# Kernel optimization log

Hardware: AMD Instinct MI355X
Metric: run time of the kernel (lower is better)

## Reference

```python
import jax, jax.numpy as jnp
import numpy as np

B, S, D, NB = 8, 8192, 512, 16


def _ln(x, g, b, eps=1e-5):
    m = jnp.mean(x, axis=-1, keepdims=True)
    v = jnp.var(x, axis=-1, keepdims=True)
    return (x - m) / jnp.sqrt(v + eps) * g + b


def setup_inputs() -> dict:
    key = jax.random.key(0)
    ks = jax.random.split(key, 12)
    s = 0.02
    f32 = jnp.float32
    return {
        "emb_input": jax.random.normal(ks[0], (B, S, D), f32),
        "dis_input": jax.random.normal(ks[1], (B, S, D), f32),
        "torsion": jax.random.normal(ks[2], (B, D), f32),
        "dis_unlocked": 1,
        "delay_steps": 3,
        # embodied selector + per-block params (stacked over NB blocks)
        "emb_sel_W": jax.random.normal(ks[3], (D, NB), f32) * s,
        "emb_sel_b": jnp.zeros((NB,), f32),
        "emb_ln_g": jnp.ones((NB, D), f32),
        "emb_ln_b": jnp.zeros((NB, D), f32),
        "emb_w1": jax.random.normal(ks[4], (NB, D, D), f32) * s,
        "emb_b1": jnp.zeros((NB, D), f32),
        "emb_w2": jax.random.normal(ks[5], (NB, D, D), f32) * s,
        "emb_b2": jnp.zeros((NB, D), f32),
        # disembodied selector + per-block params
        "dis_sel_W": jax.random.normal(ks[6], (D, NB), f32) * s,
        "dis_sel_b": jnp.zeros((NB,), f32),
        "dis_ln1_g": jnp.ones((NB, D), f32),
        "dis_ln1_b": jnp.zeros((NB, D), f32),
        "dis_attn_W": jax.random.normal(ks[7], (NB, D, D), f32) * s,
        "dis_attn_b": jnp.zeros((NB, D), f32),
        "dis_ln2_g": jnp.ones((NB, D), f32),
        "dis_ln2_b": jnp.zeros((NB, D), f32),
        "dis_ff1_W": jax.random.normal(ks[8], (NB, D, 2 * D), f32) * s,
        "dis_ff1_b": jnp.zeros((NB, 2 * D), f32),
        "dis_ff2_W": jax.random.normal(ks[9], (NB, 2 * D, D), f32) * s,
        "dis_ff2_b": jnp.zeros((NB, D), f32),
    }


def reference(emb_input, dis_input, torsion, dis_unlocked, delay_steps,
              emb_sel_W, emb_sel_b, emb_ln_g, emb_ln_b, emb_w1, emb_b1, emb_w2, emb_b2,
              dis_sel_W, dis_sel_b, dis_ln1_g, dis_ln1_b, dis_attn_W, dis_attn_b,
              dis_ln2_g, dis_ln2_b, dis_ff1_W, dis_ff1_b, dis_ff2_W, dis_ff2_b):
    # ---- embodied branch: sigmoid-gated top-2 routing (indices from batch elem 0)
    scores = jax.nn.sigmoid(jnp.mean(emb_input, axis=1) @ emb_sel_W + emb_sel_b)  # [B,NB]
    _, top = jax.lax.top_k(scores[0], 2)
    t_emb = 1.0 + torsion[:, None, :] * 0.1  # [B,1,D]
    h = emb_input
    for i in range(2):  # fixed top-2, unrolled; block params gathered dynamically
        idx = top[i]
        hn = _ln(h, emb_ln_g[idx], emb_ln_b[idx])
        hn = jnp.tanh(hn @ emb_w1[idx] + emb_b1[idx]) @ emb_w2[idx] + emb_b2[idx]
        h = h + hn * t_emb * 0.3
    emb_h = h

    # ---- disembodied branch (dis_unlocked is a static Python int)
    dis_h = None
    if dis_unlocked:
        delayed = jnp.mean(dis_input, axis=1)  # [B,D]; single-write buffer returns current mean
        dscores = jax.nn.sigmoid(delayed @ dis_sel_W + dis_sel_b)
        _, dtop = jax.lax.top_k(dscores[0], 2)
        t_dis = 1.0 + torsion[:, None, :] * 0.05
        dh = dis_input
        for i in range(2):
            idx = dtop[i]
            h1 = _ln(dh, dis_ln1_g[idx], dis_ln1_b[idx])
            h1 = h1 @ dis_attn_W[idx] + dis_attn_b[idx]
            h1 = (h1 + delayed[:, None, :] * 0.2) * t_dis
            hm = dh + h1 * 0.5
            h2 = _ln(hm, dis_ln2_g[idx], dis_ln2_b[idx])
            h2 = jax.nn.gelu(h2 @ dis_ff1_W[idx] + dis_ff1_b[idx], approximate=False)
            h2 = h2 @ dis_ff2_W[idx] + dis_ff2_b[idx]
            dh = hm + h2 * 0.5
        dis_h = dh
    return (emb_h, dis_h)
```

## Files before the change

kernel.cpp:

```cpp
#include <hip/hip_runtime.h>
#include <stdint.h>

#define B_  8
#define S_  8192
#define D_  512
#define NB_ 16
#define M_  (B_*S_)

typedef short bf16x8 __attribute__((ext_vector_type(8)));
typedef float f32x4  __attribute__((ext_vector_type(4)));

static __device__ __forceinline__ unsigned short f2bf(float f) {
  unsigned int u = __float_as_uint(f);
  u += 0x7fff + ((u >> 16) & 1);
  return (unsigned short)(u >> 16);
}

__global__ __launch_bounds__(256) void zero_kernel(float* p, int n) {
  int i = blockIdx.x * 256 + threadIdx.x;
  if (i < n) p[i] = 0.f;
}

__global__ __launch_bounds__(512) void colmean_kernel(const float* __restrict__ x,
                                                      float* __restrict__ acc) {
  int b = blockIdx.x, d = threadIdx.x;
  const float* p = x + ((size_t)b * S_ + (size_t)blockIdx.y * 512) * D_ + d;
  float s = 0.f;
  #pragma unroll 8
  for (int i = 0; i < 512; i++) s += p[(size_t)i * D_];
  atomicAdd(&acc[b * D_ + d], s);
}

__global__ __launch_bounds__(128) void top2_kernel(const float* __restrict__ embAcc,
                                                   const float* __restrict__ embW,
                                                   const float* __restrict__ embB,
                                                   const float* __restrict__ disAcc,
                                                   const float* __restrict__ disW,
                                                   const float* __restrict__ disB,
                                                   int* __restrict__ out) {
  int wave = threadIdx.x >> 6, lane = threadIdx.x & 63;
  const float* acc = wave ? disAcc : embAcc;
  const float* W   = wave ? disW   : embW;
  const float* bb  = wave ? disB   : embB;
  const float invS = 1.f / (float)S_;
  float logit[NB_];
  for (int nb = 0; nb < NB_; nb++) {
    float s = 0.f;
    for (int d = lane; d < D_; d += 64) s += acc[d] * invS * W[d * NB_ + nb];
    for (int o = 32; o; o >>= 1) s += __shfl_xor(s, o);
    logit[nb] = s + bb[nb];
  }
  if (lane == 0) {
    int i0 = 0;
    for (int i = 1; i < NB_; i++) if (logit[i] > logit[i0]) i0 = i;
    int i1 = (i0 == 0) ? 1 : 0;
    for (int i = 0; i < NB_; i++) if (i != i0 && logit[i] > logit[i1]) i1 = i;
    out[wave * 2 + 0] = i0;
    out[wave * 2 + 1] = i1;
  }
}

__global__ __launch_bounds__(256) void ln_cast_kernel(const float* __restrict__ x,
                                                      const float* __restrict__ gB,
                                                      const float* __restrict__ bB,
                                                      const int* __restrict__ idxPtr,
                                                      unsigned short* __restrict__ out) {
  int row  = blockIdx.x * 4 + (threadIdx.x >> 6);
  int lane = threadIdx.x & 63;
  const float4* xr = (const float4*)(x + (size_t)row * D_ + lane * 8);
  float4 v0 = xr[0], v1 = xr[1];
  float s  = v0.x + v0.y + v0.z + v0.w + v1.x + v1.y + v1.z + v1.w;
  float sq = v0.x*v0.x + v0.y*v0.y + v0.z*v0.z + v0.w*v0.w
           + v1.x*v1.x + v1.y*v1.y + v1.z*v1.z + v1.w*v1.w;
  for (int o = 32; o; o >>= 1) { s += __shfl_xor(s, o); sq += __shfl_xor(sq, o); }
  float mean = s * (1.f / D_);
  float var  = sq * (1.f / D_) - mean * mean;
  float rstd = rsqrtf(var + 1e-5f);
  int idx = *idxPtr;
  const float4* g4 = (const float4*)(gB + (size_t)idx * D_ + lane * 8);
  const float4* b4 = (const float4*)(bB + (size_t)idx * D_ + lane * 8);
  float4 g0 = g4[0], g1 = g4[1], c0 = b4[0], c1 = b4[1];
  float xv[8] = {v0.x, v0.y, v0.z, v0.w, v1.x, v1.y, v1.z, v1.w};
  float gv[8] = {g0.x, g0.y, g0.z, g0.w, g1.x, g1.y, g1.z, g1.w};
  float bv[8] = {c0.x, c0.y, c0.z, c0.w, c1.x, c1.y, c1.z, c1.w};
  unsigned short o8[8] __attribute__((aligned(16)));
  #pragma unroll
  for (int k = 0; k < 8; k++) o8[k] = f2bf((xv[k] - mean) * rstd * gv[k] + bv[k]);
  *(uint4*)(out + (size_t)row * D_ + lane * 8) = *(const uint4*)o8;
}

__global__ __launch_bounds__(256) void wconvert_kernel(const float* __restrict__ srcAll,
                                                       const int* __restrict__ idxPtr,
                                                       int K, int N,
                                                       unsigned short* __restrict__ dst) {
  __shared__ float t[32][33];
  int idx = *idxPtr;
  const float* src = srcAll + (size_t)idx * K * N;
  int k0 = blockIdx.y * 32, n0 = blockIdx.x * 32;
  int tid = threadIdx.x;
  int kl = tid >> 5, nl = tid & 31;
  #pragma unroll
  for (int r = 0; r < 4; r++)
    t[kl + r * 8][nl] = src[(size_t)(k0 + kl + r * 8) * N + n0 + nl];
  __syncthreads();
  #pragma unroll
  for (int r = 0; r < 4; r++)
    dst[(size_t)(n0 + kl + r * 8) * K + k0 + nl] = f2bf(t[nl][kl + r * 8]);
}

template<int EPI>
__global__ __launch_bounds__(256) void gemm_kernel(const unsigned short* __restrict__ A,
                                                   const unsigned short* __restrict__ Bt,
                                                   int K, int N,
                                                   const int* __restrict__ idxPtr,
                                                   const float* __restrict__ biasBase,
                                                   const float* __restrict__ hin,
                                                   float* __restrict__ fout,
                                                   unsigned short* __restrict__ bout,
                                                   const float* __restrict__ torsion,
                                                   const float* __restrict__ dAcc) {
  __shared__ __align__(16) unsigned short As[128 * 32];
  __shared__ __align__(16) unsigned short Bs[128 * 32];
  const int tid  = threadIdx.x;
  const int wave = tid >> 6, lane = tid & 63;
  const int quad = lane >> 4, l16 = lane & 15;
  const int wm = (wave >> 1) * 64, wn = (wave & 1) * 64;
  const int m0 = blockIdx.x * 128, n0 = blockIdx.y * 128;
  const int r0  = tid >> 2;
  const int seg = (tid & 3) * 8;
  const unsigned short* Ag = A  + (size_t)(m0 + r0) * K + seg;
  const unsigned short* Bg = Bt + (size_t)(n0 + r0) * K + seg;

  f32x4 acc[4][4] = {};
  for (int kt = 0; kt < K; kt += 32) {
    uint4 a0 = *(const uint4*)(Ag + kt);
    uint4 a1 = *(const uint4*)(Ag + (size_t)64 * K + kt);
    uint4 b0 = *(const uint4*)(Bg + kt);
    uint4 b1 = *(const uint4*)(Bg + (size_t)64 * K + kt);
    *(uint4*)(&As[(size_t)r0 * 32 + seg])        = a0;
    *(uint4*)(&As[(size_t)(r0 + 64) * 32 + seg]) = a1;
    *(uint4*)(&Bs[(size_t)r0 * 32 + seg])        = b0;
    *(uint4*)(&Bs[(size_t)(r0 + 64) * 32 + seg]) = b1;
    __syncthreads();
    bf16x8 af[4], bfr[4];
    #pragma unroll
    for (int i = 0; i < 4; i++)
      af[i] = *(const bf16x8*)(&As[(size_t)(wm + i * 16 + l16) * 32 + quad * 8]);
    #pragma unroll
    for (int j = 0; j < 4; j++)
      bfr[j] = *(const bf16x8*)(&Bs[(size_t)(wn + j * 16 + l16) * 32 + quad * 8]);
    #pragma unroll
    for (int i = 0; i < 4; i++)
      #pragma unroll
      for (int j = 0; j < 4; j++)
        acc[i][j] = __builtin_amdgcn_mfma_f32_16x16x32_bf16(af[i], bfr[j], acc[i][j], 0, 0, 0);
    __syncthreads();
  }

  const int idx = *idxPtr;
  const float* bias = biasBase + (size_t)idx * N;
  const float invS = 1.f / (float)S_;
  #pragma unroll
  for (int i = 0; i < 4; i++) {
    int rowb = m0 + wm + i * 16 + quad * 4;
    #pragma unroll
    for (int j = 0; j < 4; j++) {
      int col = n0 + wn + j * 16 + l16;
      float bc = bias[col];
      #pragma unroll
      for (int r = 0; r < 4; r++) {
        int row = rowb + r;
        size_t off = (size_t)row * N + col;
        float v = acc[i][j][r] + bc;
        if constexpr (EPI == 0) {
          bout[off] = f2bf(tanhf(v));
        } else if constexpr (EPI == 1) {
          int b = row >> 13;
          float t = 1.f + 0.1f * torsion[b * D_ + col];
          fout[off] = hin[off] + v * t * 0.3f;
        } else if constexpr (EPI == 2) {
          int b = row >> 13;
          float t = 1.f + 0.05f * torsion[b * D_ + col];
          float h1 = (v + 0.2f * dAcc[b * D_ + col] * invS) * t;
          fout[off] = hin[off] + 0.5f * h1;
        } else if constexpr (EPI == 3) {
          float gl = 0.5f * v * (1.f + erff(v * 0.70710678118654752f));
          bout[off] = f2bf(gl);
        } else {
          fout[off] = hin[off] + 0.5f * v;
        }
      }
    }
  }
}

extern "C" void kernel_launch(void* const* d_in, const int* in_sizes, int n_in,
                              void* d_out, int out_size, void* d_ws, size_t ws_size,
                              hipStream_t stream) {
  const float* emb_input  = (const float*)d_in[0];
  const float* dis_input  = (const float*)d_in[1];
  const float* torsion    = (const float*)d_in[2];
  const float* emb_sel_W  = (const float*)d_in[5];
  const float* emb_sel_b  = (const float*)d_in[6];
  const float* emb_ln_g   = (const float*)d_in[7];
  const float* emb_ln_b   = (const float*)d_in[8];
  const float* emb_w1     = (const float*)d_in[9];
  const float* emb_b1     = (const float*)d_in[10];
  const float* emb_w2     = (const float*)d_in[11];
  const float* emb_b2     = (const float*)d_in[12];
  const float* dis_sel_W  = (const float*)d_in[13];
  const float* dis_sel_b  = (const float*)d_in[14];
  const float* dis_ln1_g  = (const float*)d_in[15];
  const float* dis_ln1_b  = (const float*)d_in[16];
  const float* dis_attn_W = (const float*)d_in[17];
  const float* dis_attn_b = (const float*)d_in[18];
  const float* dis_ln2_g  = (const float*)d_in[19];
  const float* dis_ln2_b  = (const float*)d_in[20];
  const float* dis_ff1_W  = (const float*)d_in[21];
  const float* dis_ff1_b  = (const float*)d_in[22];
  const float* dis_ff2_W  = (const float*)d_in[23];
  const float* dis_ff2_b  = (const float*)d_in[24];

  char* w = (char*)d_ws;
  float* accE = (float*)w;
  float* accD = (float*)(w + 16384);
  int*   top  = (int*)(w + 32768);
  size_t o = 33024;
  unsigned short* w1t   = (unsigned short*)(w + o); o += 524288;
  unsigned short* w2t   = (unsigned short*)(w + o); o += 524288;
  unsigned short* attnT = (unsigned short*)(w + o); o += 524288;
  unsigned short* ff1T  = (unsigned short*)(w + o); o += 1048576;
  unsigned short* ff2T  = (unsigned short*)(w + o); o += 1048576;
  unsigned short* Abuf  = (unsigned short*)(w + o); o += (size_t)M_ * D_ * 2;
  unsigned short* T1    = (unsigned short*)(w + o); o += (size_t)M_ * D_ * 2;

  float* outEmb = (float*)d_out;
  float* outDis = outEmb + (size_t)M_ * D_;
  unsigned short* Gbuf = (unsigned short*)d_out;

  zero_kernel<<<32, 256, 0, stream>>>(accE, 2 * B_ * D_);
  colmean_kernel<<<dim3(1, 16), 512, 0, stream>>>(emb_input, accE);
  colmean_kernel<<<dim3(8, 16), 512, 0, stream>>>(dis_input, accD);
  top2_kernel<<<1, 128, 0, stream>>>(accE, emb_sel_W, emb_sel_b,
                                     accD, dis_sel_W, dis_sel_b, top);

  for (int s = 0; s < 2; s++) {
    const int* di = top + 2 + s;
    const float* dh = (s == 0) ? dis_input : outDis;
    wconvert_kernel<<<dim3(16, 16), 256, 0, stream>>>(dis_attn_W, di, 512, 512, attnT);
    wconvert_kernel<<<dim3(32, 16), 256, 0, stream>>>(dis_ff1_W,  di, 512, 1024, ff1T);
    wconvert_kernel<<<dim3(16, 32), 256, 0, stream>>>(dis_ff2_W,  di, 1024, 512, ff2T);
    ln_cast_kernel<<<M_ / 4, 256, 0, stream>>>(dh, dis_ln1_g, dis_ln1_b, di, Abuf);
    gemm_kernel<2><<<dim3(512, 4), 256, 0, stream>>>(Abuf, attnT, 512, 512, di,
        dis_attn_b, dh, outDis, nullptr, torsion, accD);
    ln_cast_kernel<<<M_ / 4, 256, 0, stream>>>(outDis, dis_ln2_g, dis_ln2_b, di, Abuf);
    gemm_kernel<3><<<dim3(512, 8), 256, 0, stream>>>(Abuf, ff1T, 512, 1024, di,
        dis_ff1_b, nullptr, nullptr, Gbuf, nullptr, nullptr);
    gemm_kernel<4><<<dim3(512, 4), 256, 0, stream>>>(Gbuf, ff2T, 1024, 512, di,
        dis_ff2_b, outDis, outDis, nullptr, nullptr, nullptr);
  }

  for (int s = 0; s < 2; s++) {
    const int* ei = top + s;
    const float* h = (s == 0) ? emb_input : outEmb;
    wconvert_kernel<<<dim3(16, 16), 256, 0, stream>>>(emb_w1, ei, 512, 512, w1t);
    wconvert_kernel<<<dim3(16, 16), 256, 0, stream>>>(emb_w2, ei, 512, 512, w2t);
    ln_cast_kernel<<<M_ / 4, 256, 0, stream>>>(h, emb_ln_g, emb_ln_b, ei, Abuf);
    gemm_kernel<0><<<dim3(512, 4), 256, 0, stream>>>(Abuf, w1t, 512, 512, ei,
        emb_b1, nullptr, nullptr, T1, nullptr, nullptr);
    gemm_kernel<1><<<dim3(512, 4), 256, 0, stream>>>(T1, w2t, 512, 512, ei,
        emb_b2, h, outEmb, nullptr, torsion, nullptr);
  }
}
```

Baseline: 1.899 ms.

## Use direct global-to-LDS async loads, XOR-swizzled LDS layout, and XCD-aware tile remap in GEMM

The GEMM tile loads now use global_load_lds 16-byte transfers straight into shared memory instead of staging through registers. The LDS layout gets an XOR swizzle on the k-segment so fragment reads avoid bank conflicts. The 2D grid becomes a 1D grid whose block index is remapped so consecutive tiles land on the same XCD, which should improve L2 reuse of A and B. This depends on global_load_lds with 16-byte width being supported and on the swizzle matching between writes and reads. The loop is still single-buffered, so no loads overlap with compute.

```diff
diff --git a/kernel.cpp b/kernel.cpp
--- a/kernel.cpp
+++ b/kernel.cpp
@@ -14,6 +14,15 @@
   unsigned int u = __float_as_uint(f);
   u += 0x7fff + ((u >> 16) & 1);
   return (unsigned short)(u >> 16);
+}
+
+static __device__ __forceinline__ void async_copy16(const unsigned short* g,
+                                                    unsigned short* l) {
+  auto* g1 = reinterpret_cast<const __attribute__((address_space(1))) uint32_t*>(
+      reinterpret_cast<uintptr_t>(g));
+  auto* l3 = reinterpret_cast<__attribute__((address_space(3))) uint32_t*>(
+      reinterpret_cast<uintptr_t>(l));
+  __builtin_amdgcn_global_load_lds(g1, l3, 16, 0, 0);
 }
 
 __global__ __launch_bounds__(256) void zero_kernel(float* p, int n) {
@@ -125,30 +134,41 @@
   const int wave = tid >> 6, lane = tid & 63;
   const int quad = lane >> 4, l16 = lane & 15;
   const int wm = (wave >> 1) * 64, wn = (wave & 1) * 64;
-  const int m0 = blockIdx.x * 128, n0 = blockIdx.y * 128;
-  const int r0  = tid >> 2;
-  const int seg = (tid & 3) * 8;
-  const unsigned short* Ag = A  + (size_t)(m0 + r0) * K + seg;
-  const unsigned short* Bg = Bt + (size_t)(n0 + r0) * K + seg;
+
+  const int nT  = N >> 7;
+  const int lgn = (nT == 4) ? 2 : 3;
+  const int perX = gridDim.x >> 3;
+  const int tile = (blockIdx.x & 7) * perX + (blockIdx.x >> 3);
+  const int m0 = (tile >> lgn) * 128;
+  const int n0 = (tile & (nT - 1)) * 128;
+
+  const int lrow  = lane >> 2;
+  const int segSw = (((lane & 3) ^ ((lane >> 3) & 3)) * 8);
+  const unsigned short* AgLo = A  + (size_t)(m0 + wave * 16 + lrow) * K + segSw;
+  const unsigned short* AgHi = AgLo + (size_t)64 * K;
+  const unsigned short* BgLo = Bt + (size_t)(n0 + wave * 16 + lrow) * K + segSw;
+  const unsigned short* BgHi = BgLo + (size_t)64 * K;
+  unsigned short* AsLo = &As[(wave * 16) * 32];
+  unsigned short* AsHi = &As[(wave * 16 + 64) * 32];
+  unsigned short* BsLo = &Bs[(wave * 16) * 32];
+  unsigned short* BsHi = &Bs[(wave * 16 + 64) * 32];
+
+  const int rsw = (l16 >> 1) & 3;
 
   f32x4 acc[4][4] = {};
   for (int kt = 0; kt < K; kt += 32) {
-    uint4 a0 = *(const uint4*)(Ag + kt);
-    uint4 a1 = *(const uint4*)(Ag + (size_t)64 * K + kt);
-    uint4 b0 = *(const uint4*)(Bg + kt);
-    uint4 b1 = *(const uint4*)(Bg + (size_t)64 * K + kt);
-    *(uint4*)(&As[(size_t)r0 * 32 + seg])        = a0;
-    *(uint4*)(&As[(size_t)(r0 + 64) * 32 + seg]) = a1;
-    *(uint4*)(&Bs[(size_t)r0 * 32 + seg])        = b0;
-    *(uint4*)(&Bs[(size_t)(r0 + 64) * 32 + seg]) = b1;
+    async_copy16(AgLo + kt, AsLo);
+    async_copy16(AgHi + kt, AsHi);
+    async_copy16(BgLo + kt, BsLo);
+    async_copy16(BgHi + kt, BsHi);
     __syncthreads();
     bf16x8 af[4], bfr[4];
     #pragma unroll
     for (int i = 0; i < 4; i++)
-      af[i] = *(const bf16x8*)(&As[(size_t)(wm + i * 16 + l16) * 32 + quad * 8]);
+      af[i] = *(const bf16x8*)(&As[(size_t)(wm + i * 16 + l16) * 32 + (quad ^ rsw) * 8]);
     #pragma unroll
     for (int j = 0; j < 4; j++)
-      bfr[j] = *(const bf16x8*)(&Bs[(size_t)(wn + j * 16 + l16) * 32 + quad * 8]);
+      bfr[j] = *(const bf16x8*)(&Bs[(size_t)(wn + j * 16 + l16) * 32 + (quad ^ rsw) * 8]);
     #pragma unroll
     for (int i = 0; i < 4; i++)
       #pragma unroll
@@ -251,12 +271,12 @@
     wconvert_kernel<<<dim3(32, 16), 256, 0, stream>>>(dis_ff1_W,  di, 512, 1024, ff1T);
     wconvert_kernel<<<dim3(16, 32), 256, 0, stream>>>(dis_ff2_W,  di, 1024, 512, ff2T);
     ln_cast_kernel<<<M_ / 4, 256, 0, stream>>>(dh, dis_ln1_g, dis_ln1_b, di, Abuf);
-    gemm_kernel<2><<<dim3(512, 4), 256, 0, stream>>>(Abuf, attnT, 512, 512, di,
+    gemm_kernel<2><<<2048, 256, 0, stream>>>(Abuf, attnT, 512, 512, di,
         dis_attn_b, dh, outDis, nullptr, torsion, accD);
     ln_cast_kernel<<<M_ / 4, 256, 0, stream>>>(outDis, dis_ln2_g, dis_ln2_b, di, Abuf);
-    gemm_kernel<3><<<dim3(512, 8), 256, 0, stream>>>(Abuf, ff1T, 512, 1024, di,
+    gemm_kernel<3><<<4096, 256, 0, stream>>>(Abuf, ff1T, 512, 1024, di,
         dis_ff1_b, nullptr, nullptr, Gbuf, nullptr, nullptr);
-    gemm_kernel<4><<<dim3(512, 4), 256, 0, stream>>>(Gbuf, ff2T, 1024, 512, di,
+    gemm_kernel<4><<<2048, 256, 0, stream>>>(Gbuf, ff2T, 1024, 512, di,
         dis_ff2_b, outDis, outDis, nullptr, nullptr, nullptr);
   }
 
@@ -266,9 +286,9 @@
     wconvert_kernel<<<dim3(16, 16), 256, 0, stream>>>(emb_w1, ei, 512, 512, w1t);
     wconvert_kernel<<<dim3(16, 16), 256, 0, stream>>>(emb_w2, ei, 512, 512, w2t);
     ln_cast_kernel<<<M_ / 4, 256, 0, stream>>>(h, emb_ln_g, emb_ln_b, ei, Abuf);
-    gemm_kernel<0><<<dim3(512, 4), 256, 0, stream>>>(Abuf, w1t, 512, 512, ei,
+    gemm_kernel<0><<<2048, 256, 0, stream>>>(Abuf, w1t, 512, 512, ei,
         emb_b1, nullptr, nullptr, T1, nullptr, nullptr);
-    gemm_kernel<1><<<dim3(512, 4), 256, 0, stream>>>(T1, w2t, 512, 512, ei,
+    gemm_kernel<1><<<2048, 256, 0, stream>>>(T1, w2t, 512, 512, ei,
         emb_b2, h, outEmb, nullptr, torsion, nullptr);
   }
 }
```

After: 1.811 ms. 1.05x faster.
